# Kernel tuning notes

Measured on AMD Instinct MI355X. Metric: run time of the kernel, lower is better.

Reference implementation:

```python
import jax, jax.numpy as jnp
import numpy as np

ALPHA = 0.9
CAND_LEN_LIMIT = 16
DOC_LEN_LIMIT = 256
EMBED_DIM = 768
BATCH = 8


def _tri_num(n):
    return n * (n + 1) // 2


def _build_alpha_buffers(doc_len, max_cand_len, alpha):
    """Vectorized construction of the 5 FOFE context alpha buffers.

    Candidate c = (start i, span s) enumerated by start then span, matching the
    original get_contexts_alpha_buffers ordering. end e = i + s.
      buf0 candidate ctx      : alpha^(e-j) for i <= j <= e
      buf1 left ctx excl cand : alpha^(i-1-j) for j <= i-1 (zero when i == 0)
      buf2 left ctx incl cand : alpha^(e-j) for j <= e
      buf3 right ctx excl cand: alpha^(j-1-e) for j >= e+1
      buf4 right ctx incl cand: alpha^(j-i) for j >= i
    """
    starts, spans = [], []
    for i in range(doc_len):
        n = max_cand_len if i < doc_len - max_cand_len else doc_len - i
        starts += [i] * n
        spans += list(range(n))
    s = np.asarray(starts)[:, None]              # [n_cand, 1]
    e = (np.asarray(starts) + np.asarray(spans))[:, None]
    j = np.arange(doc_len)[None, :]              # [1, doc_len]

    def pw(p, m):
        return np.where(m, alpha ** np.where(m, p, 0), 0.0).astype(np.float32)

    buf0 = pw(e - j, (j >= s) & (j <= e))
    buf1 = pw(s - 1 - j, (j <= s - 1) & (s > 0))
    buf2 = pw(e - j, j <= e)
    buf3 = pw(j - 1 - e, j >= e + 1)
    buf4 = pw(j - s, j >= s)
    cands_pos = np.concatenate([s, e], axis=1).astype(np.float32)  # [n_cand, 2]
    return (buf0, buf1, buf2, buf3, buf4), cands_pos


def setup_inputs() -> dict:
    key = jax.random.key(0)
    k1, k2 = jax.random.split(key)
    x_input = jax.random.normal(k1, (BATCH, DOC_LEN_LIMIT, EMBED_DIM), dtype=jnp.float32)
    x_mask = jax.random.randint(k2, (BATCH, DOC_LEN_LIMIT), 0, 2, dtype=jnp.int32)
    return {"x_input": x_input, "x_mask": x_mask}


def reference(x_input, x_mask):
    batch = x_input.shape[0]
    doc_len = min(x_input.shape[1], DOC_LEN_LIMIT)
    max_cand_len = min(CAND_LEN_LIMIT, doc_len)
    bufs_np, cands_pos_np = _build_alpha_buffers(doc_len, max_cand_len, ALPHA)
    buf0, buf1, buf2, buf3, buf4 = [jnp.asarray(b) for b in bufs_np]
    n_cand = buf0.shape[0]

    # concat order for has_lr_ctx_cand_incl and has_lr_ctx_cand_excl both True:
    # [left_excl, left_incl, cand, right_incl, right_excl]
    all_bufs = jnp.stack([buf1, buf2, buf0, buf4, buf3], axis=0)  # [5, n_cand, L]
    # one big contraction instead of 5 bmms
    codes = jnp.einsum('kcl,bld->bkcd', all_bufs, x_input)        # [B,5,n_cand,D]
    fofe_codes = codes.transpose(0, 2, 1, 3).reshape(batch, n_cand, 5 * x_input.shape[2])

    cands_pos = jnp.broadcast_to(jnp.asarray(cands_pos_np)[None], (batch, n_cand, 2))
    padded_cands = (jnp.einsum('cl,bl->bc', buf0, x_mask.astype(jnp.float32))[..., None] > 0)
    return fofe_codes, cands_pos, padded_cands
```

## Files before the change

kernel.cpp:

```cpp
#include <hip/hip_runtime.h>

#define NB 8
#define LEN 256
#define DIM 768
#define NC 3976
#define OFF_POS 122142720
#define OFF_PAD (122142720 + 63616)

constexpr float ALPHA_F = 0.9f;
constexpr float A32 = 0.03433683820292512f;

typedef float f4 __attribute__((ext_vector_type(4)));

__global__ __launch_bounds__(256) void scan_kernel(const float* __restrict__ x,
                                                   float* __restrict__ P,
                                                   float* __restrict__ S) {
    const int dl = threadIdx.x & 31;
    const int chunk = threadIdx.x >> 5;
    const int d = blockIdx.x * 32 + dl;
    const int b = blockIdx.y;
    const int dir = blockIdx.z;
    const float* __restrict__ xb = x + (size_t)b * LEN * DIM;
    float* __restrict__ ob = (dir ? S : P) + (size_t)b * LEN * DIM;

    float vals[32];
    float acc = 0.f;
#pragma unroll
    for (int t = 0; t < 32; ++t) {
        const int lm = chunk * 32 + t;
        const int l = dir ? (LEN - 1 - lm) : lm;
        acc = fmaf(ALPHA_F, acc, xb[l * DIM + d]);
        vals[t] = acc;
    }

    __shared__ float ends[8][32];
    ends[chunk][dl] = acc;
    __syncthreads();

    float carry = 0.f;
    for (int k = 0; k < chunk; ++k)
        carry = fmaf(A32, carry, ends[k][dl]);

    float w = ALPHA_F;
#pragma unroll
    for (int t = 0; t < 32; ++t) {
        const int lm = chunk * 32 + t;
        const int l = dir ? (LEN - 1 - lm) : lm;
        ob[l * DIM + d] = fmaf(w, carry, vals[t]);
        w *= ALPHA_F;
    }
}

__global__ __launch_bounds__(192, 4) void out_kernel(const float* __restrict__ P,
                                                     const float* __restrict__ S,
                                                     const int* __restrict__ mask,
                                                     float* __restrict__ out) {
    const int b = blockIdx.x;
    const int i = blockIdx.y;
    const int t = threadIdx.x;

    int n, c0;
    if (i <= 240) {
        n = 16;
        c0 = i * 16;
    } else {
        const int r = LEN - i;
        n = r;
        c0 = 3856 + 120 - r * (r + 1) / 2;
    }

    const f4 z4 = (f4)0.f;
    const f4* __restrict__ Pb = (const f4*)(P + (size_t)b * LEN * DIM);
    const f4* __restrict__ Sb = (const f4*)(S + (size_t)b * LEN * DIM);

    const f4 pm1 = (i > 0) ? Pb[(i - 1) * 192 + t] : z4;
    const f4 si = Sb[i * 192 + t];

    f4* o = (f4*)out + (size_t)(b * NC + c0) * 960 + t;
    float w = ALPHA_F;
    for (int s = 0; s < n; ++s) {
        const int e = i + s;
        const f4 pe = Pb[e * 192 + t];
        const f4 se1 = (e < LEN - 1) ? Sb[(e + 1) * 192 + t] : z4;
        const f4 cand = pe - w * pm1;
        o[0 * 192] = pm1;
        o[1 * 192] = pe;
        o[2 * 192] = cand;
        o[3 * 192] = si;
        o[4 * 192] = se1;
        o += 960;
        w *= ALPHA_F;
    }

    if (t < 64) {
        const int m = (t < n) ? mask[b * LEN + i + t] : 0;
        const unsigned long long ball = __ballot(m != 0);
        if (t < n) {
            const size_t c = (size_t)(b * NC + c0 + t);
            out[OFF_POS + c * 2] = (float)i;
            out[OFF_POS + c * 2 + 1] = (float)(i + t);
            out[OFF_PAD + c] = (ball & ((2ull << t) - 1)) ? 1.f : 0.f;
        }
    }
}

extern "C" void kernel_launch(void* const* d_in, const int* in_sizes, int n_in,
                              void* d_out, int out_size, void* d_ws, size_t ws_size,
                              hipStream_t stream) {
    const float* x = (const float*)d_in[0];
    const int* mask = (const int*)d_in[1];
    float* out = (float*)d_out;
    float* P = (float*)d_ws;
    float* S = P + (size_t)NB * LEN * DIM;

    scan_kernel<<<dim3(DIM / 32, NB, 2), 256, 0, stream>>>(x, P, S);
    out_kernel<<<dim3(NB, LEN), 192, 0, stream>>>(P, S, mask, out);
}
```

Before: 105.0 us.

## Replace per-start output kernel with persistent grid-stride row kernel

Result: no change. 103.2 us, median of 2 (-1.7%).

```diff
diff --git a/kernel.cpp b/kernel.cpp
--- a/kernel.cpp
+++ b/kernel.cpp
@@ -6,11 +6,19 @@
 #define NC 3976
 #define OFF_POS 122142720
 #define OFF_PAD (122142720 + 63616)
+#define NROWS (NB * NC * 5)
+#define NVROWS (NROWS + NB * LEN)
+#define NBLK 2048
 
 constexpr float ALPHA_F = 0.9f;
 constexpr float A32 = 0.03433683820292512f;
 
 typedef float f4 __attribute__((ext_vector_type(4)));
+
+__device__ __constant__ float APOW[17] = {
+    1.f, 0.9f, 0.81f, 0.729f, 0.6561f, 0.59049f, 0.531441f, 0.4782969f,
+    0.43046721f, 0.387420489f, 0.3486784401f, 0.31381059609f, 0.282429536481f,
+    0.2541865828329f, 0.22876792454961f, 0.205891132094649f, 0.1853020188851841f};
 
 __global__ __launch_bounds__(256) void scan_kernel(const float* __restrict__ x,
                                                    float* __restrict__ P,
@@ -51,55 +59,72 @@
     }
 }
 
-__global__ __launch_bounds__(192, 4) void out_kernel(const float* __restrict__ P,
-                                                     const float* __restrict__ S,
-                                                     const int* __restrict__ mask,
-                                                     float* __restrict__ out) {
-    const int b = blockIdx.x;
-    const int i = blockIdx.y;
+__global__ __launch_bounds__(192) void row_kernel(const float* __restrict__ P,
+                                                  const float* __restrict__ S,
+                                                  const int* __restrict__ mask,
+                                                  float* __restrict__ out) {
     const int t = threadIdx.x;
+    const f4* __restrict__ P4 = (const f4*)P;
+    const f4* __restrict__ S4 = (const f4*)S;
+    f4* __restrict__ out4 = (f4*)out;
 
-    int n, c0;
-    if (i <= 240) {
-        n = 16;
-        c0 = i * 16;
-    } else {
-        const int r = LEN - i;
-        n = r;
-        c0 = 3856 + 120 - r * (r + 1) / 2;
-    }
-
-    const f4 z4 = (f4)0.f;
-    const f4* __restrict__ Pb = (const f4*)(P + (size_t)b * LEN * DIM);
-    const f4* __restrict__ Sb = (const f4*)(S + (size_t)b * LEN * DIM);
-
-    const f4 pm1 = (i > 0) ? Pb[(i - 1) * 192 + t] : z4;
-    const f4 si = Sb[i * 192 + t];
-
-    f4* o = (f4*)out + (size_t)(b * NC + c0) * 960 + t;
-    float w = ALPHA_F;
-    for (int s = 0; s < n; ++s) {
-        const int e = i + s;
-        const f4 pe = Pb[e * 192 + t];
-        const f4 se1 = (e < LEN - 1) ? Sb[(e + 1) * 192 + t] : z4;
-        const f4 cand = pe - w * pm1;
-        o[0 * 192] = pm1;
-        o[1 * 192] = pe;
-        o[2 * 192] = cand;
-        o[3 * 192] = si;
-        o[4 * 192] = se1;
-        o += 960;
-        w *= ALPHA_F;
-    }
-
-    if (t < 64) {
-        const int m = (t < n) ? mask[b * LEN + i + t] : 0;
-        const unsigned long long ball = __ballot(m != 0);
-        if (t < n) {
-            const size_t c = (size_t)(b * NC + c0 + t);
-            out[OFF_POS + c * 2] = (float)i;
-            out[OFF_POS + c * 2 + 1] = (float)(i + t);
-            out[OFF_PAD + c] = (ball & ((2ull << t) - 1)) ? 1.f : 0.f;
+    for (int row = blockIdx.x; row < NVROWS; row += NBLK) {
+        if (row < NROWS) {
+            const int bc = row / 5;
+            const int which = row - bc * 5;
+            const int b = bc / NC;
+            const int c = bc - b * NC;
+            int i, s;
+            if (c < 3856) {
+                i = c >> 4;
+                s = c & 15;
+            } else {
+                const int r = c - 3856;
+                int u = 0, off = 0;
+                while (off + (15 - u) <= r) { off += 15 - u; ++u; }
+                i = 241 + u;
+                s = r - off;
+            }
+            const int e = i + s;
+            const int base = b * LEN;
+            f4 v;
+            if (which == 0) {
+                v = (i > 0) ? P4[(size_t)(base + i - 1) * 192 + t] : (f4)0.f;
+            } else if (which == 1) {
+                v = P4[(size_t)(base + e) * 192 + t];
+            } else if (which == 2) {
+                const f4 pe = P4[(size_t)(base + e) * 192 + t];
+                v = pe;
+                if (i > 0) v = pe - APOW[s + 1] * P4[(size_t)(base + i - 1) * 192 + t];
+            } else if (which == 3) {
+                v = S4[(size_t)(base + i) * 192 + t];
+            } else {
+                v = (e < LEN - 1) ? S4[(size_t)(base + e + 1) * 192 + t] : (f4)0.f;
+            }
+            out4[(size_t)row * 192 + t] = v;
+        } else {
+            const int r2 = row - NROWS;
+            const int b = r2 >> 8;
+            const int i = r2 & 255;
+            int n, c0;
+            if (i <= 240) {
+                n = 16;
+                c0 = i * 16;
+            } else {
+                const int r = LEN - i;
+                n = r;
+                c0 = 3856 + 120 - r * (r + 1) / 2;
+            }
+            if (t < 64) {
+                const int m = (t < n) ? mask[b * LEN + i + t] : 0;
+                const unsigned long long ball = __ballot(m != 0);
+                if (t < n) {
+                    const size_t c = (size_t)(b * NC + c0 + t);
+                    out[OFF_POS + c * 2] = (float)i;
+                    out[OFF_POS + c * 2 + 1] = (float)(i + t);
+                    out[OFF_PAD + c] = (ball & ((2ull << t) - 1)) ? 1.f : 0.f;
+                }
+            }
         }
     }
 }
@@ -114,5 +139,5 @@
     float* S = P + (size_t)NB * LEN * DIM;
 
     scan_kernel<<<dim3(DIM / 32, NB, 2), 256, 0, stream>>>(x, P, S);
-    out_kernel<<<dim3(NB, LEN), 192, 0, stream>>>(P, S, mask, out);
+    row_kernel<<<NBLK, 192, 0, stream>>>(P, S, mask, out);
 }
```

## Use persistent grid-stride candidate blocks with software-prefetched row loads

Applied to the files above, without the earlier changes.

Measured after the change: 111.2 us. +5.9%, slower.

```diff
diff --git a/kernel.cpp b/kernel.cpp
--- a/kernel.cpp
+++ b/kernel.cpp
@@ -4,13 +4,20 @@
 #define LEN 256
 #define DIM 768
 #define NC 3976
+#define NCAND (NB * NC)
 #define OFF_POS 122142720
 #define OFF_PAD (122142720 + 63616)
+#define NBLK 2048
 
 constexpr float ALPHA_F = 0.9f;
 constexpr float A32 = 0.03433683820292512f;
 
 typedef float f4 __attribute__((ext_vector_type(4)));
+
+__device__ __constant__ float APOW[17] = {
+    1.f, 0.9f, 0.81f, 0.729f, 0.6561f, 0.59049f, 0.531441f, 0.4782969f,
+    0.43046721f, 0.387420489f, 0.3486784401f, 0.31381059609f, 0.282429536481f,
+    0.2541865828329f, 0.22876792454961f, 0.205891132094649f, 0.1853020188851841f};
 
 __global__ __launch_bounds__(256) void scan_kernel(const float* __restrict__ x,
                                                    float* __restrict__ P,
@@ -51,57 +58,89 @@
     }
 }
 
-__global__ __launch_bounds__(192, 4) void out_kernel(const float* __restrict__ P,
-                                                     const float* __restrict__ S,
-                                                     const int* __restrict__ mask,
-                                                     float* __restrict__ out) {
-    const int b = blockIdx.x;
-    const int i = blockIdx.y;
+__global__ __launch_bounds__(192) void cand_kernel(const float* __restrict__ P,
+                                                   const float* __restrict__ S,
+                                                   const int* __restrict__ mask,
+                                                   float* __restrict__ out) {
     const int t = threadIdx.x;
+    const f4* __restrict__ P4 = (const f4*)P;
+    const f4* __restrict__ S4 = (const f4*)S;
+    f4* __restrict__ out4 = (f4*)out;
 
-    int n, c0;
-    if (i <= 240) {
-        n = 16;
-        c0 = i * 16;
-    } else {
-        const int r = LEN - i;
-        n = r;
-        c0 = 3856 + 120 - r * (r + 1) / 2;
+#define DECODE_LOAD(BC, PM1, PE, SI, SE1, SS)                               \
+    {                                                                       \
+        const int b_ = (BC) / NC;                                           \
+        const int c_ = (BC) - b_ * NC;                                      \
+        int i_, s_;                                                         \
+        if (c_ < 3856) {                                                    \
+            i_ = c_ >> 4;                                                   \
+            s_ = c_ & 15;                                                   \
+        } else {                                                            \
+            const int r_ = c_ - 3856;                                       \
+            int u_ = 0, off_ = 0;                                           \
+            while (off_ + (15 - u_) <= r_) { off_ += 15 - u_; ++u_; }       \
+            i_ = 241 + u_;                                                  \
+            s_ = r_ - off_;                                                 \
+        }                                                                   \
+        const int e_ = i_ + s_;                                             \
+        const int base_ = b_ * LEN;                                         \
+        PM1 = (i_ > 0) ? P4[(size_t)(base_ + i_ - 1) * 192 + t] : (f4)0.f;  \
+        PE = P4[(size_t)(base_ + e_) * 192 + t];                            \
+        SI = S4[(size_t)(base_ + i_) * 192 + t];                            \
+        SE1 = (e_ < LEN - 1) ? S4[(size_t)(base_ + e_ + 1) * 192 + t] : (f4)0.f; \
+        SS = s_;                                                            \
     }
 
-    const f4 z4 = (f4)0.f;
-    const f4* __restrict__ Pb = (const f4*)(P + (size_t)b * LEN * DIM);
-    const f4* __restrict__ Sb = (const f4*)(S + (size_t)b * LEN * DIM);
+    int bc = blockIdx.x;
+    f4 cpm1, cpe, csi, cse1;
+    int cs;
+    DECODE_LOAD(bc, cpm1, cpe, csi, cse1, cs);
 
-    const f4 pm1 = (i > 0) ? Pb[(i - 1) * 192 + t] : z4;
-    const f4 si = Sb[i * 192 + t];
+    for (;;) {
+        const int bn = bc + NBLK;
+        const bool hn = bn < NCAND;
+        f4 npm1, npe, nsi, nse1;
+        int ns;
+        if (hn) DECODE_LOAD(bn, npm1, npe, nsi, nse1, ns);
 
-    f4* o = (f4*)out + (size_t)(b * NC + c0) * 960 + t;
-    float w = ALPHA_F;
-    for (int s = 0; s < n; ++s) {
-        const int e = i + s;
-        const f4 pe = Pb[e * 192 + t];
-        const f4 se1 = (e < LEN - 1) ? Sb[(e + 1) * 192 + t] : z4;
-        const f4 cand = pe - w * pm1;
-        o[0 * 192] = pm1;
-        o[1 * 192] = pe;
+        const f4 cand = cpe - APOW[cs + 1] * cpm1;
+        f4* o = out4 + (size_t)bc * 960 + t;
+        o[0 * 192] = cpm1;
+        o[1 * 192] = cpe;
         o[2 * 192] = cand;
-        o[3 * 192] = si;
-        o[4 * 192] = se1;
-        o += 960;
-        w *= ALPHA_F;
+        o[3 * 192] = csi;
+        o[4 * 192] = cse1;
+
+        if (!hn) break;
+        cpm1 = npm1; cpe = npe; csi = nsi; cse1 = nse1; cs = ns;
+        bc = bn;
     }
 
-    if (t < 64) {
-        const int m = (t < n) ? mask[b * LEN + i + t] : 0;
-        const unsigned long long ball = __ballot(m != 0);
-        if (t < n) {
-            const size_t c = (size_t)(b * NC + c0 + t);
-            out[OFF_POS + c * 2] = (float)i;
-            out[OFF_POS + c * 2 + 1] = (float)(i + t);
-            out[OFF_PAD + c] = (ball & ((2ull << t) - 1)) ? 1.f : 0.f;
+    {
+        const int r2 = blockIdx.x;
+        const int b = r2 >> 8;
+        const int i = r2 & 255;
+        int n, c0;
+        if (i <= 240) {
+            n = 16;
+            c0 = i * 16;
+        } else {
+            const int r = LEN - i;
+            n = r;
+            c0 = 3856 + 120 - r * (r + 1) / 2;
+        }
+        if (t < 64) {
+            const int m = (t < n) ? mask[b * LEN + i + t] : 0;
+            const unsigned long long ball = __ballot(m != 0);
+            if (t < n) {
+                const size_t c = (size_t)(b * NC + c0 + t);
+                out[OFF_POS + c * 2] = (float)i;
+                out[OFF_POS + c * 2 + 1] = (float)(i + t);
+                out[OFF_PAD + c] = (ball & ((2ull << t) - 1)) ? 1.f : 0.f;
+            }
         }
     }
+#undef DECODE_LOAD
 }
 
 extern "C" void kernel_launch(void* const* d_in, const int* in_sizes, int n_in,
@@ -114,5 +153,5 @@
     float* S = P + (size_t)NB * LEN * DIM;
 
     scan_kernel<<<dim3(DIM / 32, NB, 2), 256, 0, stream>>>(x, P, S);
-    out_kernel<<<dim3(NB, LEN), 192, 0, stream>>>(P, S, mask, out);
+    cand_kernel<<<NBLK, 192, 0, stream>>>(P, S, mask, out);
 }
```
